# Optimization experiments

Measured on AMD Instinct MI355X. Metric: run time of the kernel, lower is better.

Reference implementation:

```python
import jax, jax.numpy as jnp
import numpy as np

B, T, J = 128, 12, 17
HID, HEADS = 128, 8
LH, NC = 512, 500
E_IN = J * HID + 2 * HID  # 2432, matches hidden_channels*19 in the torch code

_pairs = [[15,13],[13,11],[16,14],[14,12],[11,12],[5,11],[6,12],[5,6],[5,7],
          [6,8],[7,9],[8,10],[1,2],[0,1],[0,2],[1,3],[2,4],[3,5],[4,6]]
_pairs = _pairs + [[b, a] for a, b in _pairs]
CONN = np.array(_pairs, dtype=np.int32).T  # [2, 38]: row0=source, row1=target


def setup_inputs():
    key = jax.random.key(0)
    ks = iter(jax.random.split(key, 48))
    def w(shape, s=0.05):
        return jax.random.normal(next(ks), shape, dtype=jnp.float32) * s
    inp = dict(
        pose1=jax.random.normal(next(ks), (B, T, J, 3), dtype=jnp.float32),
        pose2=jax.random.normal(next(ks), (B, T, J, 3), dtype=jnp.float32),
        W1=w((3, HEADS * HID)), a_src1=w((HEADS, HID)), a_dst1=w((HEADS, HID)),
        b1=jnp.zeros((HEADS * HID,), jnp.float32),
        W2=w((HEADS * HID, HEADS * HID)), a_src2=w((HEADS, HID)), a_dst2=w((HEADS, HID)),
        b2=jnp.zeros((HID,), jnp.float32),
        W_fc=w((2 * 19, HID)), b_fc=jnp.zeros((HID,), jnp.float32),
        bn_gamma=jnp.ones((T,), jnp.float32) + w((T,), 0.1),
        bn_beta=w((T,), 0.1), bn_mean=w((T,), 0.1), bn_var=jnp.ones((T,), jnp.float32),
        Wih_f=w((4 * LH, E_IN)), Whh_f=w((4 * LH, LH)),
        bih_f=jnp.zeros((4 * LH,), jnp.float32), bhh_f=jnp.zeros((4 * LH,), jnp.float32),
        Wih_b=w((4 * LH, E_IN)), Whh_b=w((4 * LH, LH)),
        bih_b=jnp.zeros((4 * LH,), jnp.float32), bhh_b=jnp.zeros((4 * LH,), jnp.float32),
        W_att=w((1, 2 * LH)), b_att=jnp.zeros((1,), jnp.float32),
        W_cls=w((NC, 2 * LH)), b_cls=jnp.zeros((NC,), jnp.float32),
        modal=0,
    )
    return inp


def reference(pose1, pose2, W1, a_src1, a_dst1, b1, W2, a_src2, a_dst2, b2,
              W_fc, b_fc, bn_gamma, bn_beta, bn_mean, bn_var,
              Wih_f, Whh_f, bih_f, bhh_f, Wih_b, Whh_b, bih_b, bhh_b,
              W_att, b_att, W_cls, b_cls, modal):
    c0 = jnp.asarray(CONN[0])
    c1 = jnp.asarray(CONN[1])

    def gat_conv(x, W, a_s, a_d, bias, esrc, edst, N, concat):
        # PyG GATConv (eval mode): self-loops already included in esrc/edst.
        H, C = a_s.shape
        h = (x @ W).reshape(N, H, C)
        al_s = jnp.einsum('nhc,hc->nh', h, a_s)   # [N,H]
        al_d = jnp.einsum('nhc,hc->nh', h, a_d)
        e = jax.nn.leaky_relu(al_s[esrc] + al_d[edst], 0.2)          # [E,H]
        m = jax.ops.segment_max(e, edst, num_segments=N)             # softmax per target
        ex = jnp.exp(e - m[edst])
        den = jax.ops.segment_sum(ex, edst, num_segments=N)
        a = ex / den[edst]
        out = jax.ops.segment_sum(a[:, :, None] * h[esrc], edst, num_segments=N)
        return (out.reshape(N, H * C) if concat else out.mean(axis=1)) + bias

    def gat_seq(pose):  # [B,T,J,3] -> [B,T,J*HID]
        Bq, Tq = pose.shape[0], pose.shape[1]
        N = Bq * J
        loops = jnp.arange(N, dtype=c0.dtype)
        esrc = jnp.concatenate([c0, loops])
        edst = jnp.concatenate([c1, loops])
        x = pose.transpose(1, 0, 2, 3).reshape(Tq, N, 3)
        def block(xf):
            hcat = jax.nn.elu(gat_conv(xf, W1, a_src1, a_dst1, b1, esrc, edst, N, True))
            return gat_conv(hcat, W2, a_src2, a_dst2, b2, esrc, edst, N, False)
        out = jax.vmap(block)(x)  # [T, N, HID]
        return out.reshape(Tq, Bq, J * HID).transpose(1, 0, 2)

    def edge_branch(pose):  # [B,T,J,3] -> [B,T,2*HID]
        Bq, Tq = pose.shape[0], pose.shape[1]
        p = pose.reshape(-1, J, 3)
        v = p[:, c1, :2] - p[:, c0, :2]                              # [BT,38,2]
        ef = jnp.stack([jnp.linalg.norm(v, axis=-1),
                        jnp.arctan2(v[..., 1], v[..., 0])], axis=-1)  # [BT,38,2]
        ef = ef.reshape(-1, 2 * 19) @ W_fc + b_fc                    # view(-1,38): [2*BT,128]
        return ef.reshape(Bq, Tq, 2 * HID)

    if modal == 0:
        f1 = jnp.concatenate([gat_seq(pose1), edge_branch(pose1)], axis=-1)
        f2 = jnp.concatenate([gat_seq(pose2), edge_branch(pose2)], axis=-1)
        feats = jnp.concatenate([f1, f2], axis=0)
    else:
        feats = jnp.concatenate([gat_seq(pose1), edge_branch(pose1)], axis=-1)

    # BatchNorm1d(12), eval mode, channels = time dim 1
    inv = jax.lax.rsqrt(bn_var + 1e-5)
    feats = (feats - bn_mean[None, :, None]) * (inv * bn_gamma)[None, :, None] + bn_beta[None, :, None]

    def lstm_dir(x, Wih, Whh, bih, bhh, reverse):
        pre = jnp.einsum('btd,gd->btg', x, Wih) + bih + bhh
        Bq = x.shape[0]
        init = (jnp.zeros((Bq, LH), x.dtype), jnp.zeros((Bq, LH), x.dtype))
        def step(carry, xt):
            h, c = carry
            g = xt + h @ Whh.T
            i, f, gg, o = jnp.split(g, 4, axis=-1)  # torch gate order i,f,g,o
            c = jax.nn.sigmoid(f) * c + jax.nn.sigmoid(i) * jnp.tanh(gg)
            h = jax.nn.sigmoid(o) * jnp.tanh(c)
            return (h, c), h
        _, ys = jax.lax.scan(step, init, pre.transpose(1, 0, 2), reverse=reverse)
        return ys.transpose(1, 0, 2)

    lout = jnp.concatenate([
        lstm_dir(feats, Wih_f, Whh_f, bih_f, bhh_f, False),
        lstm_dir(feats, Wih_b, Whh_b, bih_b, bhh_b, True)], axis=-1)  # [2B,T,1024]

    attw = jax.nn.softmax(lout @ W_att.T + b_att, axis=1)
    attended = jnp.sum(lout * attw, axis=1)   # [2B,1024]
    logits = attended @ W_cls.T + b_cls       # [2B,NC]
    return (attended, logits)
```

## Files before the change

kernel.cpp:

```cpp
#include <hip/hip_runtime.h>
#include <hip/hip_bf16.h>
#include <math.h>

#define B_    128
#define T_    12
#define J_    17
#define HID_  128
#define LH_   512
#define NC_   500

typedef short  bf16x8 __attribute__((ext_vector_type(8)));
typedef ushort u16x8  __attribute__((ext_vector_type(8)));
typedef float  f32x4  __attribute__((ext_vector_type(4)));

__constant__ int d_c0[38] = {15,13,16,14,11,5,6,5,5,6,7,8,1,0,0,1,2,3,4,
                             13,11,14,12,12,11,12,6,7,8,9,10,2,1,2,3,4,5,6};
__constant__ int d_c1[38] = {13,11,14,12,12,11,12,6,7,8,9,10,2,1,2,3,4,5,6,
                             15,13,16,14,11,5,6,5,5,6,7,8,1,0,0,1,2,3,4};

__device__ __forceinline__ float lrelu02(float x){ return x > 0.f ? x : 0.2f*x; }
__device__ __forceinline__ float sigmoidf_(float x){ return 1.f/(1.f+__expf(-x)); }
__device__ __forceinline__ ushort f2bf(float f){
  uint32_t u = __builtin_bit_cast(uint32_t, f);
  uint32_t r = (u + 0x7fffu + ((u >> 16) & 1u)) >> 16;
  return (ushort)r;
}
__device__ __forceinline__ void llds16(const ushort* g, ushort* l){
  __builtin_amdgcn_global_load_lds(
      (const __attribute__((address_space(1))) void*)g,
      (__attribute__((address_space(3))) void*)l,
      16, 0, 0);
}

__global__ __launch_bounds__(256) void k_wprep(const float* __restrict__ W2,
    const float* __restrict__ Wih_f, const float* __restrict__ Wih_b,
    const float* __restrict__ Whh_f, const float* __restrict__ Whh_b,
    ushort* __restrict__ W2mT, ushort* __restrict__ W2tb,
    ushort* __restrict__ Wbf, ushort* __restrict__ Whh_pbf){
  __shared__ ushort sh[64][68];
  int tid = threadIdx.x;
  int bx = blockIdx.x;
  if (bx < 512){
    int idx = bx*256 + tid;
    int c = idx >> 10, k = idx & 1023;
    float s = 0.f;
    #pragma unroll
    for (int h = 0; h < 8; h++) s += W2[k*1024 + h*128 + c];
    W2mT[idx] = f2bf(s * 0.125f);
  } else if (bx < 768){
    int b2x = bx - 512;
    int k0 = (b2x >> 4)*64, n0 = (b2x & 15)*64;
    #pragma unroll
    for (int q = 0; q < 16; q++){
      int idx = tid + q*256;
      int kk = idx >> 6, nn = idx & 63;
      sh[nn][kk] = f2bf(W2[(size_t)(k0+kk)*1024 + n0+nn]);
    }
    __syncthreads();
    #pragma unroll
    for (int q = 0; q < 16; q++){
      int idx = tid + q*256;
      int nn = idx >> 6, kk = idx & 63;
      W2tb[(size_t)(n0+nn)*1024 + k0+kk] = sh[nn][kk];
    }
  } else if (bx < 10496){
    const int S = 2048*2432;
    int i4 = (bx - 768)*256 + tid;
    int idx = i4*4;
    if (idx >= 2*S) return;
    const float* src = (idx < S) ? (Wih_f + idx) : (Wih_b + (idx - S));
    float4 v = *(const float4*)src;
    ushort4 o;
    o.x = f2bf(v.x); o.y = f2bf(v.y); o.z = f2bf(v.z); o.w = f2bf(v.w);
    *(ushort4*)(Wbf + idx) = o;
  } else {
    int i = (bx - 10496)*256 + tid;
    int base = i*8;
    int dir = base >> 20;
    int rem = base & 1048575;
    int n_p = rem >> 9, k8 = rem & 511;
    int u = n_p >> 2, g = n_p & 3;
    const float* src = (dir ? Whh_b : Whh_f) + ((size_t)(g*512+u))*512 + k8;
    float4 v0 = *(const float4*)src;
    float4 v1 = *(const float4*)(src+4);
    ushort av[8] = {f2bf(v0.x),f2bf(v0.y),f2bf(v0.z),f2bf(v0.w),
                    f2bf(v1.x),f2bf(v1.y),f2bf(v1.z),f2bf(v1.w)};
    *(u16x8*)(Whh_pbf + (size_t)base) = *(u16x8*)av;
  }
}

__global__ __launch_bounds__(256) void k_gat1_special(const float* __restrict__ pose1,
    const float* __restrict__ pose2, const float* __restrict__ W1, float* __restrict__ rawh_p){
  int p = blockIdx.x / 204, r = blockIdx.x % 204;
  const float* pose = p ? pose2 : pose1;
  float* rawh = rawh_p + p*208896;
  int t = r/17, n = r%17;
  const float* xp = pose + (t*17 + n)*3;
  float x0 = xp[0], x1 = xp[1], x2 = xp[2];
  int tid = threadIdx.x;
  #pragma unroll
  for (int j = 0; j < 4; j++){
    int c = tid + j*256;
    rawh[(t*17+n)*1024 + c] = x0*W1[c] + x1*W1[1024+c] + x2*W1[2048+c];
  }
}

__global__ void k_compute_al(const float* __restrict__ hbuf_p, const float* __restrict__ a_s,
    const float* __restrict__ a_d, float* __restrict__ al_s_p, float* __restrict__ al_d_p){
  int p = blockIdx.x / 204, tn = blockIdx.x % 204;
  const float* hbuf = hbuf_p + p*208896 + tn*1024;
  int tid = threadIdx.x;
  int o = tid >> 4, l = tid & 15;
  int h = o & 7;
  const float* av = ((o < 8) ? a_s : a_d) + h*128;
  const float* hv = hbuf + h*128;
  float s = 0.f;
  #pragma unroll
  for (int q = 0; q < 8; q++) s += hv[l + q*16] * av[l + q*16];
  #pragma unroll
  for (int off = 1; off < 16; off <<= 1) s += __shfl_xor(s, off, 64);
  if (l == 0) ((o < 8) ? al_s_p : al_d_p)[p*2048 + tn*8 + h] = s;
}

__global__ __launch_bounds__(256) void k_gat1_agg(const float* __restrict__ rawh_p,
    const float* __restrict__ al_s_p, const float* __restrict__ al_d_p,
    const float* __restrict__ b1, ushort* __restrict__ hcat_bf){
  int p = blockIdx.x / 204, r = blockIdx.x % 204;
  const float* rawh = rawh_p + p*208896;
  const float* al_s = al_s_p + p*2048;
  const float* al_d = al_d_p + p*2048;
  int t = r/17, dst = r%17;
  int base = t*17, tid = threadIdx.x;
  int row = p*204 + base + dst;
  #pragma unroll
  for (int j = 0; j < 4; j++){
    int c = tid + j*256, h = c >> 7;
    float ad = al_d[(base+dst)*8 + h];
    float eself = lrelu02(al_s[(base+dst)*8 + h] + ad);
    float m = eself;
    for (int e = 0; e < 38; e++) if (d_c1[e] == dst)
      m = fmaxf(m, lrelu02(al_s[(base+d_c0[e])*8 + h] + ad));
    float w = __expf(eself - m);
    float den = w;
    float acc = w * rawh[(base+dst)*1024 + c];
    for (int e = 0; e < 38; e++) if (d_c1[e] == dst){
      float v = __expf(lrelu02(al_s[(base+d_c0[e])*8 + h] + ad) - m);
      den += v;
      acc += v * rawh[(base+d_c0[e])*1024 + c];
    }
    float o = acc/den + b1[c];
    hcat_bf[(size_t)row*1024 + c] = f2bf(o > 0.f ? o : __expf(o) - 1.f);
  }
}

#define GLDK 40
__global__ __launch_bounds__(256) void k_gat2m(
    const float* __restrict__ pose1, const float* __restrict__ pose2,
    const float* __restrict__ W1, const float* __restrict__ b1,
    const ushort* __restrict__ W2mT, const float* __restrict__ b2,
    const float* __restrict__ bn_g, const float* __restrict__ bn_b,
    const float* __restrict__ bn_m, const float* __restrict__ bn_v,
    ushort* __restrict__ fb)
{
  int t = blockIdx.y;
  int p = blockIdx.z;
  const float* pose = p ? pose2 : pose1;
  int n0 = blockIdx.x * 64;
  __shared__ ushort As[64*GLDK];
  __shared__ ushort Bs[128*GLDK];
  __shared__ float sx[64][3];
  int tid = threadIdx.x;
  if (tid < 192){
    int nd = tid/3, k = tid%3;
    int n = n0+nd, b = n/17, jj = n%17;
    sx[nd][k] = pose[((b*12 + t)*17 + jj)*3 + k];
  }
  __syncthreads();
  float inv = rsqrtf(bn_v[t] + 1e-5f);
  float sc = inv*bn_g[t], shv = bn_b[t] - bn_m[t]*sc;
  int wave = tid >> 6, lane = tid & 63;
  int wm = (wave >> 1)*32, wn = (wave & 1)*64;
  int fr = lane & 15, fg = lane >> 4;
  int and_ = tid >> 2, ak8 = (tid & 3)*8;
  int brow = tid >> 1, bk16 = (tid & 1)*16;
  float ax0 = sx[and_][0], ax1 = sx[and_][1], ax2 = sx[and_][2];

  f32x4 acc[2][4];
  #pragma unroll
  for (int m = 0; m < 2; m++)
    #pragma unroll
    for (int n = 0; n < 4; n++) acc[m][n] = (f32x4){0.f,0.f,0.f,0.f};

  for (int k0 = 0; k0 < 1024; k0 += 32){
    if (k0) __syncthreads();
    {
      ushort av[8];
      #pragma unroll
      for (int q = 0; q < 8; q++){
        int k = k0 + ak8 + q;
        float hv = ax0*W1[k] + ax1*W1[1024+k] + ax2*W1[2048+k] + b1[k];
        hv = hv > 0.f ? hv : __expf(hv) - 1.f;
        av[q] = f2bf(hv);
      }
      *(u16x8*)(&As[and_*GLDK + ak8]) = *(u16x8*)av;
    }
    *(u16x8*)(&Bs[brow*GLDK + bk16])     = *(const u16x8*)(W2mT + brow*1024 + k0 + bk16);
    *(u16x8*)(&Bs[brow*GLDK + bk16 + 8]) = *(const u16x8*)(W2mT + brow*1024 + k0 + bk16 + 8);
    __syncthreads();
    bf16x8 af[2], bfv[4];
    #pragma unroll
    for (int m = 0; m < 2; m++)
      af[m] = *(const bf16x8*)(&As[(wm + m*16 + fr)*GLDK + fg*8]);
    #pragma unroll
    for (int n = 0; n < 4; n++)
      bfv[n] = *(const bf16x8*)(&Bs[(wn + n*16 + fr)*GLDK + fg*8]);
    #pragma unroll
    for (int m = 0; m < 2; m++)
      #pragma unroll
      for (int n = 0; n < 4; n++)
        acc[m][n] = __builtin_amdgcn_mfma_f32_16x16x32_bf16(af[m], bfv[n], acc[m][n], 0, 0, 0);
  }

  #pragma unroll
  for (int m = 0; m < 2; m++){
    #pragma unroll
    for (int n = 0; n < 4; n++){
      int col = wn + n*16 + fr;
      float bb = b2[col];
      #pragma unroll
      for (int j = 0; j < 4; j++){
        int node = n0 + wm + m*16 + fg*4 + j;
        int b = node/17, jj = node%17;
        float val = (acc[m][n][j] + bb)*sc + shv;
        fb[(((size_t)(p*128+b))*12 + t)*2432 + jj*128 + col] = f2bf(val);
      }
    }
  }
}

#define PLDK 40
__global__ __launch_bounds__(256) void k_gat2sp(
    const ushort* __restrict__ hcat_bf,
    const ushort* __restrict__ W2tb,
    float* __restrict__ h2s)
{
  __shared__ ushort As[64*PLDK];
  __shared__ ushort Bs[128*PLDK];
  int tid = threadIdx.x;
  int bm = blockIdx.y * 64;
  int bn = blockIdx.x * 128;
  int wave = tid >> 6, lane = tid & 63;
  int wm = (wave >> 1)*32, wn = (wave & 1)*64;
  int fr = lane & 15, fg = lane >> 4;
  int arow = tid >> 2, ak8 = (tid & 3)*8;
  int brow = tid >> 1, bk16 = (tid & 1)*16;

  f32x4 acc[2][4];
  #pragma unroll
  for (int m = 0; m < 2; m++)
    #pragma unroll
    for (int n = 0; n < 4; n++) acc[m][n] = (f32x4){0.f,0.f,0.f,0.f};

  for (int k0 = 0; k0 < 1024; k0 += 32){
    if (k0) __syncthreads();
    *(u16x8*)(&As[arow*PLDK + ak8]) = *(const u16x8*)(hcat_bf + (size_t)(bm+arow)*1024 + k0 + ak8);
    *(u16x8*)(&Bs[brow*PLDK + bk16])     = *(const u16x8*)(W2tb + (size_t)(bn+brow)*1024 + k0 + bk16);
    *(u16x8*)(&Bs[brow*PLDK + bk16 + 8]) = *(const u16x8*)(W2tb + (size_t)(bn+brow)*1024 + k0 + bk16 + 8);
    __syncthreads();
    bf16x8 af[2], bfv[4];
    #pragma unroll
    for (int m = 0; m < 2; m++)
      af[m] = *(const bf16x8*)(&As[(wm + m*16 + fr)*PLDK + fg*8]);
    #pragma unroll
    for (int n = 0; n < 4; n++)
      bfv[n] = *(const bf16x8*)(&Bs[(wn + n*16 + fr)*PLDK + fg*8]);
    #pragma unroll
    for (int m = 0; m < 2; m++)
      #pragma unroll
      for (int n = 0; n < 4; n++)
        acc[m][n] = __builtin_amdgcn_mfma_f32_16x16x32_bf16(af[m], bfv[n], acc[m][n], 0, 0, 0);
  }

  #pragma unroll
  for (int m = 0; m < 2; m++){
    #pragma unroll
    for (int n = 0; n < 4; n++){
      int col = bn + wn + n*16 + fr;
      #pragma unroll
      for (int j = 0; j < 4; j++){
        int row = bm + wm + m*16 + fg*4 + j;
        if (row < 408) h2s[(size_t)row*1024 + col] = acc[m][n][j];
      }
    }
  }
}

__global__ void k_gat2_agg(const float* __restrict__ h2s_p, const float* __restrict__ al_s_p,
    const float* __restrict__ al_d_p, const float* __restrict__ b2,
    const float* __restrict__ bn_g, const float* __restrict__ bn_b,
    const float* __restrict__ bn_m, const float* __restrict__ bn_v,
    ushort* __restrict__ fb){
  int p = blockIdx.x / 204, r = blockIdx.x % 204;
  const float* h2s = h2s_p + p*208896;
  const float* al_s = al_s_p + p*2048;
  const float* al_d = al_d_p + p*2048;
  int t = r/17, dst = r%17;
  int base = t*17, c = threadIdx.x;
  float sum = 0.f;
  for (int h = 0; h < 8; h++){
    float ad = al_d[(base+dst)*8 + h];
    float eself = lrelu02(al_s[(base+dst)*8 + h] + ad);
    float m = eself;
    for (int e = 0; e < 38; e++) if (d_c1[e] == dst)
      m = fmaxf(m, lrelu02(al_s[(base+d_c0[e])*8 + h] + ad));
    float w = __expf(eself - m), den = w;
    float acc = w * h2s[(base+dst)*1024 + h*128 + c];
    for (int e = 0; e < 38; e++) if (d_c1[e] == dst){
      float v = __expf(lrelu02(al_s[(base+d_c0[e])*8 + h] + ad) - m);
      den += v;
      acc += v * h2s[(base+d_c0[e])*1024 + h*128 + c];
    }
    sum += acc/den;
  }
  float inv = rsqrtf(bn_v[t] + 1e-5f);
  float sc = inv*bn_g[t], shv = bn_b[t] - bn_m[t]*sc;
  float val = (sum*0.125f + b2[c])*sc + shv;
  fb[(((size_t)(p*128))*12 + t)*2432 + dst*128 + c] = f2bf(val);
}

__global__ __launch_bounds__(256) void k_edge_branch(const float* __restrict__ pose1,
    const float* __restrict__ pose2, const float* __restrict__ W_fc,
    const float* __restrict__ b_fc,
    const float* __restrict__ bn_g, const float* __restrict__ bn_b,
    const float* __restrict__ bn_m, const float* __restrict__ bn_v,
    ushort* __restrict__ fb){
  int p = blockIdx.x / 1536, bt = blockIdx.x % 1536;
  const float* pose = p ? pose2 : pose1;
  int b = bt/12, t = bt%12;
  __shared__ float nrm[38], ang[38];
  int tid = threadIdx.x;
  if (tid < 38){
    const float* pb = pose + ((b*12 + t)*17)*3;
    int s = d_c0[tid], d = d_c1[tid];
    float vx = pb[d*3+0] - pb[s*3+0];
    float vy = pb[d*3+1] - pb[s*3+1];
    nrm[tid] = sqrtf(vx*vx + vy*vy);
    ang[tid] = atan2f(vy, vx);
  }
  __syncthreads();
  float inv = rsqrtf(bn_v[t] + 1e-5f);
  float sc = inv*bn_g[t], shv = bn_b[t] - bn_m[t]*sc;
  int c = tid & 127, blk = tid >> 7;
  float acc = b_fc[c];
  #pragma unroll
  for (int j = 0; j < 19; j++){
    int e = blk*19 + j;
    acc += nrm[e]*W_fc[(2*j)*128 + c] + ang[e]*W_fc[(2*j+1)*128 + c];
  }
  fb[(((size_t)(p*128+b))*12 + t)*2432 + 2176 + blk*128 + c] = f2bf(acc*sc + shv);
}

__global__ __launch_bounds__(256) void k_proj_mfma(
    const ushort* __restrict__ Abf,
    const ushort* __restrict__ Wbf,
    const float* __restrict__ bih_f, const float* __restrict__ bhh_f,
    const float* __restrict__ bih_b, const float* __restrict__ bhh_b,
    float* __restrict__ pre)
{
  __shared__ ushort As[128*32];
  __shared__ ushort Bs[128*32];
  int tid = threadIdx.x;
  int bm = blockIdx.y * 128;
  int dir = blockIdx.x >> 4;
  int bn = (blockIdx.x & 15) * 128;
  const ushort* W = Wbf + (size_t)dir * (2048*2432);
  const float* bi = dir ? bih_b : bih_f;
  const float* bh = dir ? bhh_b : bhh_f;
  float* C = pre + (size_t)dir * 6291456;

  int wave = tid >> 6, lane = tid & 63;
  int wm = (wave >> 1) * 64, wn = (wave & 1) * 64;
  int fr = lane & 15, fg = lane >> 4;

  int grow = tid >> 2, gks = (tid & 3) * 8;
  const ushort* gaBase = Abf + (size_t)(bm + grow)*2432 + gks;
  const ushort* gbBase = W   + (size_t)(bn + grow)*2432 + gks;
  ushort* ldsA0 = &As[(wave*16)*32];
  ushort* ldsA1 = &As[(64 + wave*16)*32];
  ushort* ldsB0 = &Bs[(wave*16)*32];
  ushort* ldsB1 = &Bs[(64 + wave*16)*32];

  f32x4 acc[4][4];
  #pragma unroll
  for (int i = 0; i < 4; i++)
    #pragma unroll
    for (int j = 0; j < 4; j++) acc[i][j] = (f32x4){0.f,0.f,0.f,0.f};

  for (int k0 = 0; k0 < 2432; k0 += 32){
    __syncthreads();
    llds16(gaBase + k0,             ldsA0);
    llds16(gaBase + k0 + 64*2432,   ldsA1);
    llds16(gbBase + k0,             ldsB0);
    llds16(gbBase + k0 + 64*2432,   ldsB1);
    __syncthreads();
    bf16x8 af[4], bfv[4];
    #pragma unroll
    for (int m = 0; m < 4; m++)
      af[m] = *(const bf16x8*)(&As[(wm + m*16 + fr)*32 + fg*8]);
    #pragma unroll
    for (int n = 0; n < 4; n++)
      bfv[n] = *(const bf16x8*)(&Bs[(wn + n*16 + fr)*32 + fg*8]);
    #pragma unroll
    for (int m = 0; m < 4; m++)
      #pragma unroll
      for (int n = 0; n < 4; n++)
        acc[m][n] = __builtin_amdgcn_mfma_f32_16x16x32_bf16(af[m], bfv[n], acc[m][n], 0, 0, 0);
  }

  #pragma unroll
  for (int m = 0; m < 4; m++){
    #pragma unroll
    for (int n = 0; n < 4; n++){
      int col = bn + wn + n*16 + fr;
      float bsum = bi[col] + bh[col];
      #pragma unroll
      for (int j = 0; j < 4; j++){
        int row = bm + wm + m*16 + fg*4 + j;
        C[(size_t)row*2048 + col] = acc[m][n][j] + bsum;
      }
    }
  }
}

#define SLDK 40
__global__ __launch_bounds__(256) void k_lstm_step(
    ushort* __restrict__ hbf, const ushort* __restrict__ Whh_pbf,
    const float* __restrict__ pre, float* __restrict__ cbuf,
    float* __restrict__ lout, int s)
{
  int dir = blockIdx.z;
  int bm = blockIdx.y * 64;
  int bn = blockIdx.x * 64;
  int tCur = dir ? (11 - s) : s;
  int tid = threadIdx.x, wave = tid >> 6, lane = tid & 63;
  int fr = lane & 15, fg = lane >> 4;
  __shared__ ushort As[64*SLDK];
  __shared__ ushort Bs[64*SLDK];
  __shared__ float sg[64][68];
  f32x4 acc[4];
  #pragma unroll
  for (int n = 0; n < 4; n++) acc[n] = (f32x4){0.f,0.f,0.f,0.f};

  if (s > 0){
    const ushort* hA = hbf + ((size_t)((s&1)*2 + dir))*131072;
    const ushort* WB = Whh_pbf + (size_t)dir*1048576;
    int srow = tid >> 2, sk8 = (tid & 3)*8;
    for (int k0 = 0; k0 < 512; k0 += 32){
      if (k0) __syncthreads();
      *(u16x8*)(&As[srow*SLDK + sk8]) = *(const u16x8*)(hA + (size_t)(bm+srow)*512 + k0 + sk8);
      *(u16x8*)(&Bs[srow*SLDK + sk8]) = *(const u16x8*)(WB + (size_t)(bn+srow)*512 + k0 + sk8);
      __syncthreads();
      bf16x8 af = *(const bf16x8*)(&As[(wave*16 + fr)*SLDK + fg*8]);
      #pragma unroll
      for (int n = 0; n < 4; n++){
        bf16x8 bfv = *(const bf16x8*)(&Bs[(n*16 + fr)*SLDK + fg*8]);
        acc[n] = __builtin_amdgcn_mfma_f32_16x16x32_bf16(af, bfv, acc[n], 0, 0, 0);
      }
    }
  }
  #pragma unroll
  for (int n = 0; n < 4; n++)
    #pragma unroll
    for (int j = 0; j < 4; j++)
      sg[wave*16 + fg*4 + j][n*16 + fr] = acc[n][j];
  __syncthreads();

  int ul = tid & 15, rb = tid >> 4;
  int u = (bn >> 2) + ul;
  ushort* hw = hbf + ((size_t)(((s&1)^1)*2 + dir))*131072;
  #pragma unroll
  for (int q = 0; q < 4; q++){
    int r = rb + q*16, b = bm + r;
    const float* pb = pre + (size_t)dir*6291456 + ((size_t)b*12 + tCur)*2048;
    float gi = sg[r][ul*4+0] + pb[u];
    float gf = sg[r][ul*4+1] + pb[512+u];
    float gg = sg[r][ul*4+2] + pb[1024+u];
    float go = sg[r][ul*4+3] + pb[1536+u];
    float cP = (s > 0) ? cbuf[dir*131072 + b*512 + u] : 0.f;
    float cN = sigmoidf_(gf)*cP + sigmoidf_(gi)*tanhf(gg);
    float h = sigmoidf_(go)*tanhf(cN);
    cbuf[dir*131072 + b*512 + u] = cN;
    lout[((size_t)b*12 + tCur)*1024 + dir*512 + u] = h;
    hw[(size_t)b*512 + u] = f2bf(h);
  }
}

__global__ __launch_bounds__(256) void k_gemm_bt(
    const float* __restrict__ A, int lda,
    const float* __restrict__ B, int ldb,
    float* __restrict__ C, int ldc,
    int M, int N, int K,
    const float* __restrict__ bias1)
{
  __shared__ float As[16][68];
  __shared__ float Bs[16][68];
  int tid = threadIdx.x;
  int bm = blockIdx.y*64, bn = blockIdx.x*64;
  int lr = tid >> 2, lk = (tid & 3) << 2;
  int tx = tid & 15, ty = tid >> 4;
  float acc[4][4] = {{0.f}};
  for (int k0 = 0; k0 < K; k0 += 16){
    float4 va = make_float4(0.f,0.f,0.f,0.f), vb = make_float4(0.f,0.f,0.f,0.f);
    int ar = bm + lr;
    if (ar < M) va = *(const float4*)(A + (size_t)ar*lda + k0 + lk);
    int br = bn + lr;
    if (br < N) vb = *(const float4*)(B + (size_t)br*ldb + k0 + lk);
    As[lk+0][lr]=va.x; As[lk+1][lr]=va.y; As[lk+2][lr]=va.z; As[lk+3][lr]=va.w;
    Bs[lk+0][lr]=vb.x; Bs[lk+1][lr]=vb.y; Bs[lk+2][lr]=vb.z; Bs[lk+3][lr]=vb.w;
    __syncthreads();
    #pragma unroll
    for (int kk = 0; kk < 16; kk++){
      float4 av = *(const float4*)(&As[kk][ty*4]);
      float4 bv = *(const float4*)(&Bs[kk][tx*4]);
      acc[0][0] += av.x*bv.x; acc[0][1] += av.x*bv.y; acc[0][2] += av.x*bv.z; acc[0][3] += av.x*bv.w;
      acc[1][0] += av.y*bv.x; acc[1][1] += av.y*bv.y; acc[1][2] += av.y*bv.z; acc[1][3] += av.y*bv.w;
      acc[2][0] += av.z*bv.x; acc[2][1] += av.z*bv.y; acc[2][2] += av.z*bv.z; acc[2][3] += av.z*bv.w;
      acc[3][0] += av.w*bv.x; acc[3][1] += av.w*bv.y; acc[3][2] += av.w*bv.z; acc[3][3] += av.w*bv.w;
    }
    __syncthreads();
  }
  #pragma unroll
  for (int i = 0; i < 4; i++){
    int r = bm + ty*4 + i;
    if (r >= M) continue;
    #pragma unroll
    for (int j = 0; j < 4; j++){
      int cc = bn + tx*4 + j;
      if (cc >= N) continue;
      float v = acc[i][j];
      if (bias1) v += bias1[cc];
      C[(size_t)r*ldc + cc] = v;
    }
  }
}

__global__ __launch_bounds__(256) void k_attention(const float* __restrict__ lout,
    const float* __restrict__ W_att, float* __restrict__ attended){
  int b = blockIdx.x, tid = threadIdx.x;
  __shared__ float part[256*12];
  __shared__ float sc[12];
  float p[12];
  #pragma unroll
  for (int t = 0; t < 12; t++) p[t] = 0.f;
  #pragma unroll
  for (int j = 0; j < 4; j++){
    int c = tid + j*256;
    float w = W_att[c];
    #pragma unroll
    for (int t = 0; t < 12; t++) p[t] += lout[((size_t)b*12 + t)*1024 + c] * w;
  }
  #pragma unroll
  for (int t = 0; t < 12; t++) part[tid*12 + t] = p[t];
  __syncthreads();
  if (tid < 12){
    float s = 0.f;
    for (int i = 0; i < 256; i++) s += part[i*12 + tid];
    sc[tid] = s;
  }
  __syncthreads();
  float m = sc[0];
  #pragma unroll
  for (int t = 1; t < 12; t++) m = fmaxf(m, sc[t]);
  float wt[12], den = 0.f;
  #pragma unroll
  for (int t = 0; t < 12; t++){ wt[t] = __expf(sc[t] - m); den += wt[t]; }
  float inv = 1.f/den;
  #pragma unroll
  for (int j = 0; j < 4; j++){
    int c = tid + j*256;
    float a = 0.f;
    #pragma unroll
    for (int t = 0; t < 12; t++) a += wt[t]*lout[((size_t)b*12 + t)*1024 + c];
    attended[(size_t)b*1024 + c] = a*inv;
  }
}

extern "C" void kernel_launch(void* const* d_in, const int* in_sizes, int n_in,
                              void* d_out, int out_size, void* d_ws, size_t ws_size,
                              hipStream_t stream)
{
  const float* pose1 = (const float*)d_in[0];
  const float* pose2 = (const float*)d_in[1];
  const float* W1    = (const float*)d_in[2];
  const float* a_src1= (const float*)d_in[3];
  const float* a_dst1= (const float*)d_in[4];
  const float* b1    = (const float*)d_in[5];
  const float* W2    = (const float*)d_in[6];
  const float* a_src2= (const float*)d_in[7];
  const float* a_dst2= (const float*)d_in[8];
  const float* b2    = (const float*)d_in[9];
  const float* W_fc  = (const float*)d_in[10];
  const float* b_fc  = (const float*)d_in[11];
  const float* bn_g  = (const float*)d_in[12];
  const float* bn_b  = (const float*)d_in[13];
  const float* bn_m  = (const float*)d_in[14];
  const float* bn_v  = (const float*)d_in[15];
  const float* Wih_f = (const float*)d_in[16];
  const float* Whh_f = (const float*)d_in[17];
  const float* bih_f = (const float*)d_in[18];
  const float* bhh_f = (const float*)d_in[19];
  const float* Wih_b = (const float*)d_in[20];
  const float* Whh_b = (const float*)d_in[21];
  const float* bih_b = (const float*)d_in[22];
  const float* bhh_b = (const float*)d_in[23];
  const float* W_att = (const float*)d_in[24];
  const float* W_cls = (const float*)d_in[26];
  const float* b_cls = (const float*)d_in[27];
  (void)in_sizes; (void)n_in; (void)out_size; (void)ws_size;

  float* ws = (float*)d_ws;
  ushort* Wbf     = (ushort*)ws;
  ushort* Whh_pbf = (ushort*)(ws + 4980736);
  ushort* W2tb    = (ushort*)(ws + 6029312);
  ushort* W2mT    = (ushort*)(ws + 6553600);
  float* pre      = ws + 7471104;
  float* R        = ws + 20054016;
  ushort* fb      = (ushort*)R;
  float* rawh_p   = R;
  float* h2s      = R + 3735552;
  ushort* hcat_bf = (ushort*)(R + 4153344);
  float* alB      = R + 4382720;
  float* al1s = alB, *al1d = alB + 4096, *al2s = alB + 8192, *al2d = alB + 12288;
  ushort* hbf = (ushort*)R;
  float* cbuf = R + 262144;
  float* lout = R + 524288;

  float* attended = (float*)d_out;
  float* logits   = attended + 262144;

  k_wprep<<<11520, 256, 0, stream>>>(W2, Wih_f, Wih_b, Whh_f, Whh_b,
                                     W2mT, W2tb, Wbf, Whh_pbf);

  k_gat1_special<<<408, 256, 0, stream>>>(pose1, pose2, W1, rawh_p);
  k_compute_al<<<408, 256, 0, stream>>>(rawh_p, a_src1, a_dst1, al1s, al1d);
  k_gat1_agg<<<408, 256, 0, stream>>>(rawh_p, al1s, al1d, b1, hcat_bf);
  k_gat2m<<<dim3(34,12,2), 256, 0, stream>>>(pose1, pose2, W1, b1, W2mT, b2,
                                             bn_g, bn_b, bn_m, bn_v, fb);
  k_gat2sp<<<dim3(8,7), 256, 0, stream>>>(hcat_bf, W2tb, h2s);
  k_compute_al<<<408, 256, 0, stream>>>(h2s, a_src2, a_dst2, al2s, al2d);
  k_gat2_agg<<<408, 128, 0, stream>>>(h2s, al2s, al2d, b2,
                                      bn_g, bn_b, bn_m, bn_v, fb);
  k_edge_branch<<<3072, 256, 0, stream>>>(pose1, pose2, W_fc, b_fc,
                                          bn_g, bn_b, bn_m, bn_v, fb);

  k_proj_mfma<<<dim3(32, 24), 256, 0, stream>>>(fb, Wbf,
      bih_f, bhh_f, bih_b, bhh_b, pre);

  for (int s = 0; s < 12; s++)
    k_lstm_step<<<dim3(32,4,2), 256, 0, stream>>>(hbf, Whh_pbf, pre, cbuf, lout, s);

  k_attention<<<256, 256, 0, stream>>>(lout, W_att, attended);
  k_gemm_bt<<<dim3(8,4), 256, 0, stream>>>(attended, 1024, W_cls, 1024, logits, 500,
                                           256, 500, 1024, b_cls);
}
```

Measured before the change: 431.0 us.

## Split LSTM step K across two wave groups, fuse GAT1 attention logits, prefetch GEMM tiles

The LSTM recurrence kernel now uses 512 threads: two groups of four waves each take half of the K dimension, load tiles with llds16, and combine their partial sums in shared memory. The aim is to cut per-step latency on the serial 12-step chain. Separately, the GAT1 projection is fused with the attention-logit dot products through shared memory, which removes one launch and a global re-read. The two GAT2 GEMMs also prefetch the next K-slice from global memory into registers. The extra syncs and the reduction add overhead, and the shared-memory tiles lose their padding, which may cause bank conflicts.

```diff
diff --git a/kernel.cpp b/kernel.cpp
--- a/kernel.cpp
+++ b/kernel.cpp
@@ -89,20 +89,35 @@
   }
 }
 
-__global__ __launch_bounds__(256) void k_gat1_special(const float* __restrict__ pose1,
-    const float* __restrict__ pose2, const float* __restrict__ W1, float* __restrict__ rawh_p){
-  int p = blockIdx.x / 204, r = blockIdx.x % 204;
+__global__ __launch_bounds__(256) void k_gat1s_al(const float* __restrict__ pose1,
+    const float* __restrict__ pose2, const float* __restrict__ W1,
+    const float* __restrict__ a_s, const float* __restrict__ a_d,
+    float* __restrict__ rawh_p, float* __restrict__ al_s_p, float* __restrict__ al_d_p){
+  __shared__ float rh[1024];
+  int p = blockIdx.x / 204, tn = blockIdx.x % 204;
   const float* pose = p ? pose2 : pose1;
   float* rawh = rawh_p + p*208896;
-  int t = r/17, n = r%17;
-  const float* xp = pose + (t*17 + n)*3;
+  const float* xp = pose + tn*3;
   float x0 = xp[0], x1 = xp[1], x2 = xp[2];
   int tid = threadIdx.x;
   #pragma unroll
   for (int j = 0; j < 4; j++){
     int c = tid + j*256;
-    rawh[(t*17+n)*1024 + c] = x0*W1[c] + x1*W1[1024+c] + x2*W1[2048+c];
-  }
+    float v = x0*W1[c] + x1*W1[1024+c] + x2*W1[2048+c];
+    rh[c] = v;
+    rawh[tn*1024 + c] = v;
+  }
+  __syncthreads();
+  int o = tid >> 4, l = tid & 15;
+  int h = o & 7;
+  const float* av = ((o < 8) ? a_s : a_d) + h*128;
+  const float* hv = rh + h*128;
+  float s = 0.f;
+  #pragma unroll
+  for (int q = 0; q < 8; q++) s += hv[l + q*16] * av[l + q*16];
+  #pragma unroll
+  for (int off = 1; off < 16; off <<= 1) s += __shfl_xor(s, off, 64);
+  if (l == 0) ((o < 8) ? al_s_p : al_d_p)[p*2048 + tn*8 + h] = s;
 }
 
 __global__ void k_compute_al(const float* __restrict__ hbuf_p, const float* __restrict__ a_s,
@@ -191,22 +206,27 @@
     #pragma unroll
     for (int n = 0; n < 4; n++) acc[m][n] = (f32x4){0.f,0.f,0.f,0.f};
 
+  u16x8 vb0 = *(const u16x8*)(W2mT + brow*1024 + bk16);
+  u16x8 vb1 = *(const u16x8*)(W2mT + brow*1024 + bk16 + 8);
+
   for (int k0 = 0; k0 < 1024; k0 += 32){
+    ushort av[8];
+    #pragma unroll
+    for (int q = 0; q < 8; q++){
+      int k = k0 + ak8 + q;
+      float hv = ax0*W1[k] + ax1*W1[1024+k] + ax2*W1[2048+k] + b1[k];
+      hv = hv > 0.f ? hv : __expf(hv) - 1.f;
+      av[q] = f2bf(hv);
+    }
     if (k0) __syncthreads();
-    {
-      ushort av[8];
-      #pragma unroll
-      for (int q = 0; q < 8; q++){
-        int k = k0 + ak8 + q;
-        float hv = ax0*W1[k] + ax1*W1[1024+k] + ax2*W1[2048+k] + b1[k];
-        hv = hv > 0.f ? hv : __expf(hv) - 1.f;
-        av[q] = f2bf(hv);
-      }
-      *(u16x8*)(&As[and_*GLDK + ak8]) = *(u16x8*)av;
-    }
-    *(u16x8*)(&Bs[brow*GLDK + bk16])     = *(const u16x8*)(W2mT + brow*1024 + k0 + bk16);
-    *(u16x8*)(&Bs[brow*GLDK + bk16 + 8]) = *(const u16x8*)(W2mT + brow*1024 + k0 + bk16 + 8);
+    *(u16x8*)(&As[and_*GLDK + ak8]) = *(u16x8*)av;
+    *(u16x8*)(&Bs[brow*GLDK + bk16])     = vb0;
+    *(u16x8*)(&Bs[brow*GLDK + bk16 + 8]) = vb1;
     __syncthreads();
+    if (k0 + 32 < 1024){
+      vb0 = *(const u16x8*)(W2mT + brow*1024 + k0 + 32 + bk16);
+      vb1 = *(const u16x8*)(W2mT + brow*1024 + k0 + 32 + bk16 + 8);
+    }
     bf16x8 af[2], bfv[4];
     #pragma unroll
     for (int m = 0; m < 2; m++)
@@ -261,12 +281,23 @@
     #pragma unroll
     for (int n = 0; n < 4; n++) acc[m][n] = (f32x4){0.f,0.f,0.f,0.f};
 
+  const ushort* ga = hcat_bf + (size_t)(bm+arow)*1024 + ak8;
+  const ushort* gb = W2tb + (size_t)(bn+brow)*1024 + bk16;
+  u16x8 va  = *(const u16x8*)ga;
+  u16x8 vb0 = *(const u16x8*)gb;
+  u16x8 vb1 = *(const u16x8*)(gb + 8);
+
   for (int k0 = 0; k0 < 1024; k0 += 32){
     if (k0) __syncthreads();
-    *(u16x8*)(&As[arow*PLDK + ak8]) = *(const u16x8*)(hcat_bf + (size_t)(bm+arow)*1024 + k0 + ak8);
-    *(u16x8*)(&Bs[brow*PLDK + bk16])     = *(const u16x8*)(W2tb + (size_t)(bn+brow)*1024 + k0 + bk16);
-    *(u16x8*)(&Bs[brow*PLDK + bk16 + 8]) = *(const u16x8*)(W2tb + (size_t)(bn+brow)*1024 + k0 + bk16 + 8);
+    *(u16x8*)(&As[arow*PLDK + ak8]) = va;
+    *(u16x8*)(&Bs[brow*PLDK + bk16])     = vb0;
+    *(u16x8*)(&Bs[brow*PLDK + bk16 + 8]) = vb1;
     __syncthreads();
+    if (k0 + 32 < 1024){
+      va  = *(const u16x8*)(ga + k0 + 32);
+      vb0 = *(const u16x8*)(gb + k0 + 32);
+      vb1 = *(const u16x8*)(gb + k0 + 40);
+    }
     bf16x8 af[2], bfv[4];
     #pragma unroll
     for (int m = 0; m < 2; m++)
@@ -432,8 +463,7 @@
   }
 }
 
-#define SLDK 40
-__global__ __launch_bounds__(256) void k_lstm_step(
+__global__ __launch_bounds__(512) void k_lstm_step(
     ushort* __restrict__ hbf, const ushort* __restrict__ Whh_pbf,
     const float* __restrict__ pre, float* __restrict__ cbuf,
     float* __restrict__ lout, int s)
@@ -443,9 +473,10 @@
   int bn = blockIdx.x * 64;
   int tCur = dir ? (11 - s) : s;
   int tid = threadIdx.x, wave = tid >> 6, lane = tid & 63;
+  int kg = wave >> 2, wv = wave & 3;
   int fr = lane & 15, fg = lane >> 4;
-  __shared__ ushort As[64*SLDK];
-  __shared__ ushort Bs[64*SLDK];
+  __shared__ ushort As[2][64*32];
+  __shared__ ushort Bs[2][64*32];
   __shared__ float sg[64][68];
   f32x4 acc[4];
   #pragma unroll
@@ -454,33 +485,48 @@
   if (s > 0){
     const ushort* hA = hbf + ((size_t)((s&1)*2 + dir))*131072;
     const ushort* WB = Whh_pbf + (size_t)dir*1048576;
-    int srow = tid >> 2, sk8 = (tid & 3)*8;
-    for (int k0 = 0; k0 < 512; k0 += 32){
+    int rsub = lane >> 2, kl = (lane & 3)*8;
+    const ushort* gA = hA + (size_t)(bm + wv*16 + rsub)*512 + kg*256 + kl;
+    const ushort* gB = WB + (size_t)(bn + wv*16 + rsub)*512 + kg*256 + kl;
+    ushort* lA = &As[kg][(wv*16)*32];
+    ushort* lB = &Bs[kg][(wv*16)*32];
+    for (int k0 = 0; k0 < 256; k0 += 32){
       if (k0) __syncthreads();
-      *(u16x8*)(&As[srow*SLDK + sk8]) = *(const u16x8*)(hA + (size_t)(bm+srow)*512 + k0 + sk8);
-      *(u16x8*)(&Bs[srow*SLDK + sk8]) = *(const u16x8*)(WB + (size_t)(bn+srow)*512 + k0 + sk8);
+      llds16(gA + k0, lA);
+      llds16(gB + k0, lB);
       __syncthreads();
-      bf16x8 af = *(const bf16x8*)(&As[(wave*16 + fr)*SLDK + fg*8]);
+      bf16x8 af = *(const bf16x8*)(&As[kg][(wv*16 + fr)*32 + fg*8]);
       #pragma unroll
       for (int n = 0; n < 4; n++){
-        bf16x8 bfv = *(const bf16x8*)(&Bs[(n*16 + fr)*SLDK + fg*8]);
+        bf16x8 bfv = *(const bf16x8*)(&Bs[kg][(n*16 + fr)*32 + fg*8]);
         acc[n] = __builtin_amdgcn_mfma_f32_16x16x32_bf16(af, bfv, acc[n], 0, 0, 0);
       }
     }
-  }
-  #pragma unroll
-  for (int n = 0; n < 4; n++)
-    #pragma unroll
-    for (int j = 0; j < 4; j++)
-      sg[wave*16 + fg*4 + j][n*16 + fr] = acc[n][j];
+    __syncthreads();
+  }
+  if (kg == 0){
+    #pragma unroll
+    for (int n = 0; n < 4; n++)
+      #pragma unroll
+      for (int j = 0; j < 4; j++)
+        sg[wv*16 + fg*4 + j][n*16 + fr] = acc[n][j];
+  }
+  __syncthreads();
+  if (kg == 1){
+    #pragma unroll
+    for (int n = 0; n < 4; n++)
+      #pragma unroll
+      for (int j = 0; j < 4; j++)
+        sg[wv*16 + fg*4 + j][n*16 + fr] += acc[n][j];
+  }
   __syncthreads();
 
   int ul = tid & 15, rb = tid >> 4;
   int u = (bn >> 2) + ul;
   ushort* hw = hbf + ((size_t)(((s&1)^1)*2 + dir))*131072;
   #pragma unroll
-  for (int q = 0; q < 4; q++){
-    int r = rb + q*16, b = bm + r;
+  for (int q = 0; q < 2; q++){
+    int r = rb + q*32, b = bm + r;
     const float* pb = pre + (size_t)dir*6291456 + ((size_t)b*12 + tCur)*2048;
     float gi = sg[r][ul*4+0] + pb[u];
     float gf = sg[r][ul*4+1] + pb[512+u];
@@ -641,8 +687,8 @@
   k_wprep<<<11520, 256, 0, stream>>>(W2, Wih_f, Wih_b, Whh_f, Whh_b,
                                      W2mT, W2tb, Wbf, Whh_pbf);
 
-  k_gat1_special<<<408, 256, 0, stream>>>(pose1, pose2, W1, rawh_p);
-  k_compute_al<<<408, 256, 0, stream>>>(rawh_p, a_src1, a_dst1, al1s, al1d);
+  k_gat1s_al<<<408, 256, 0, stream>>>(pose1, pose2, W1, a_src1, a_dst1,
+                                      rawh_p, al1s, al1d);
   k_gat1_agg<<<408, 256, 0, stream>>>(rawh_p, al1s, al1d, b1, hcat_bf);
   k_gat2m<<<dim3(34,12,2), 256, 0, stream>>>(pose1, pose2, W1, b1, W2mT, b2,
                                              bn_g, bn_b, bn_m, bn_v, fb);
@@ -657,7 +703,7 @@
       bih_f, bhh_f, bih_b, bhh_b, pre);
 
   for (int s = 0; s < 12; s++)
-    k_lstm_step<<<dim3(32,4,2), 256, 0, stream>>>(hbf, Whh_pbf, pre, cbuf, lout, s);
+    k_lstm_step<<<dim3(32,4,2), 512, 0, stream>>>(hbf, Whh_pbf, pre, cbuf, lout, s);
 
   k_attention<<<256, 256, 0, stream>>>(lout, W_att, attended);
   k_gemm_bt<<<dim3(8,4), 256, 0, stream>>>(attended, 1024, W_cls, 1024, logits, 500,
```

Result: faster. 398.4 us (-7.6%).
